# Performance work log

Hardware: AMD Instinct MI355X
Metric: run time of the kernel (lower is better)

## Reference

```python
import jax, jax.numpy as jnp
import numpy as np

H = 1024
NH = 16
HD = H // NH  # 64


def setup_inputs() -> dict:
    key = jax.random.key(0)
    ks = jax.random.split(key, 7)
    s = 1.0 / np.sqrt(H)
    return {
        "hidden_states": jax.random.normal(ks[0], (4, 2048, H), dtype=jnp.float32),
        "Wq": jax.random.normal(ks[1], (H, H), dtype=jnp.float32) * s,
        "bq": jnp.zeros((H,), dtype=jnp.float32),
        "Wk": jax.random.normal(ks[2], (H, H), dtype=jnp.float32) * s,
        "bk": jnp.zeros((H,), dtype=jnp.float32),
        "Wv": jax.random.normal(ks[3], (H, H), dtype=jnp.float32) * s,
        "bv": jnp.zeros((H,), dtype=jnp.float32),
    }


def _split_heads(x):
    # [B,S,H] -> [B,NH,S,HD]
    b, s, _ = x.shape
    return x.reshape(b, s, NH, HD).transpose(0, 2, 1, 3)


def reference(hidden_states, Wq, bq, Wk, bk, Wv, bv):
    q = _split_heads(hidden_states @ Wq + bq)
    k = _split_heads(hidden_states @ Wk + bk)
    v = _split_heads(hidden_states @ Wv + bv)
    scores = jnp.einsum("bhqd,bhkd->bhqk", q, k) / jnp.sqrt(jnp.float32(HD))
    probs = jax.nn.softmax(scores, axis=-1)  # dropout p=0 (eval) -> identity
    ctx = jnp.einsum("bhqk,bhkd->bhqd", probs, v)
    b, _, s, _ = ctx.shape
    return ctx.transpose(0, 2, 1, 3).reshape(b, s, H)
```

## Files before the change

### kernel.cpp

```cpp
#include <hip/hip_runtime.h>
#include <hip/hip_bf16.h>

#define BB  4
#define SS  2048
#define HH  1024
#define NHH 16
#define HDD 64

typedef unsigned short u16;
typedef unsigned int   u32;
using bf16x8 = __attribute__((ext_vector_type(8))) short;
using f32x4  = __attribute__((ext_vector_type(4))) float;
using f32x16 = __attribute__((ext_vector_type(16))) float;
using u32x4  = __attribute__((ext_vector_type(4))) u32;

#define SBAR()   asm volatile("s_barrier" ::: "memory")
#define WAITV0() asm volatile("s_waitcnt vmcnt(0)" ::: "memory")
#define WAITV4() asm volatile("s_waitcnt vmcnt(4)" ::: "memory")
#define WAITV8() asm volatile("s_waitcnt vmcnt(8)" ::: "memory")
#define SCHEDB() __builtin_amdgcn_sched_barrier(0)

__device__ __forceinline__ u16 f2b(float f) {
    union { float f; u32 u; } x; x.f = f;
    return (u16)((x.u + 0x7fffu + ((x.u >> 16) & 1u)) >> 16);
}

__device__ __forceinline__ void gload16(const u16* g, u16* l) {
    __builtin_amdgcn_global_load_lds(
        (const __attribute__((address_space(1))) void*)g,
        (__attribute__((address_space(3))) void*)l, 16, 0, 0);
}

__global__ __launch_bounds__(256) void conv(
    const float* __restrict__ X,
    const float* __restrict__ Wq, const float* __restrict__ Wk,
    const float* __restrict__ Wv,
    u16* __restrict__ Xb, u16* __restrict__ Wt)
{
    const int bid = blockIdx.x;
    const int t = threadIdx.x;
    if (bid < 4096) {
        const int i = bid * 256 + t;
        float4 a = ((const float4*)X)[i * 2];
        float4 b = ((const float4*)X)[i * 2 + 1];
        ushort4 s0, s1;
        s0.x = f2b(a.x); s0.y = f2b(a.y); s0.z = f2b(a.z); s0.w = f2b(a.w);
        s1.x = f2b(b.x); s1.y = f2b(b.y); s1.z = f2b(b.z); s1.w = f2b(b.w);
        ((ushort4*)Xb)[i * 2] = s0;
        ((ushort4*)Xb)[i * 2 + 1] = s1;
        return;
    }
    const int idx = bid - 4096;
    const int z = idx >> 10, rem = idx & 1023;
    const int k0 = (rem >> 5) * 32, n0 = (rem & 31) * 32;
    const float* W = (z == 0) ? Wq : (z == 1) ? Wk : Wv;
    u16* out = Wt + (size_t)z * HH * HH;
    __shared__ float T[32][33];
    {
        const int kl = t >> 3, n4 = (t & 7) * 4;
        float4 v = *(const float4*)&W[(size_t)(k0 + kl) * HH + n0 + n4];
        T[n4 + 0][kl] = v.x; T[n4 + 1][kl] = v.y;
        T[n4 + 2][kl] = v.z; T[n4 + 3][kl] = v.w;
    }
    __syncthreads();
    {
        const int nl = t >> 3, k4 = (t & 7) * 4;
        ushort4 s;
        s.x = f2b(T[nl][k4 + 0]); s.y = f2b(T[nl][k4 + 1]);
        s.z = f2b(T[nl][k4 + 2]); s.w = f2b(T[nl][k4 + 3]);
        *(ushort4*)&out[(size_t)(n0 + nl) * HH + k0 + k4] = s;
    }
}

__global__ __launch_bounds__(256, 2) void qkv_gemm(
    const u16* __restrict__ Xb, const u16* __restrict__ Wtb,
    const float* __restrict__ bq, const float* __restrict__ bk,
    const float* __restrict__ bv,
    u16* __restrict__ Qw, u16* __restrict__ Kw, u16* __restrict__ Vw)
{
    const int z  = blockIdx.z;
    const float* bias = (z == 0) ? bq : (z == 1) ? bk : bv;
    const int m0 = blockIdx.x * 128, n0 = blockIdx.y * 128;

    __shared__ __align__(16) u16 Xs[2][128 * 64];
    __shared__ __align__(16) u16 Ws[2][128 * 64];

    const int t = threadIdx.x;
    const int w = t >> 6, lane = t & 63, lr = lane & 15, quad = lane >> 4;
    const int l3 = lane >> 3, c7 = lane & 7;
    const int cl = (c7 ^ l3) * 8;
    const int wm = w >> 1, wn = w & 1;

    const u16* Wtz = Wtb + (size_t)z * HH * HH;

    f32x4 acc[4][4];
    #pragma unroll
    for (int i = 0; i < 4; i++)
        #pragma unroll
        for (int j = 0; j < 4; j++) acc[i][j] = f32x4{0.f, 0.f, 0.f, 0.f};

    #pragma unroll
    for (int e = 0; e < 4; e++) {
        const int r = w * 32 + e * 8 + l3;
        gload16(&Xb [(size_t)(m0 + r) * HH + cl], &Xs[0][(w * 32 + e * 8) * 64]);
        gload16(&Wtz[(size_t)(n0 + r) * HH + cl], &Ws[0][(w * 32 + e * 8) * 64]);
    }

    for (int kt = 0; kt < 16; kt++) {
        const int cur = kt & 1;
        if (kt < 15) {
            const int k0 = (kt + 1) * 64;
            #pragma unroll
            for (int e = 0; e < 4; e++) {
                const int r = w * 32 + e * 8 + l3;
                gload16(&Xb [(size_t)(m0 + r) * HH + k0 + cl],
                        &Xs[cur ^ 1][(w * 32 + e * 8) * 64]);
                gload16(&Wtz[(size_t)(n0 + r) * HH + k0 + cl],
                        &Ws[cur ^ 1][(w * 32 + e * 8) * 64]);
            }
            WAITV8();
        } else {
            WAITV0();
        }
        SBAR();
        SCHEDB();

        #pragma unroll
        for (int kc = 0; kc < 2; kc++) {
            bf16x8 af[4], bfr[4];
            const int ph = ((kc * 4 + quad) ^ c7) * 8;
            #pragma unroll
            for (int mi = 0; mi < 4; mi++)
                af[mi] = *(const bf16x8*)&Xs[cur][(wm * 64 + mi * 16 + lr) * 64 + ph];
            #pragma unroll
            for (int ni = 0; ni < 4; ni++)
                bfr[ni] = *(const bf16x8*)&Ws[cur][(wn * 64 + ni * 16 + lr) * 64 + ph];
            if (z != 2) {
                #pragma unroll
                for (int mi = 0; mi < 4; mi++)
                    #pragma unroll
                    for (int ni = 0; ni < 4; ni++)
                        acc[mi][ni] = __builtin_amdgcn_mfma_f32_16x16x32_bf16(
                            bfr[ni], af[mi], acc[mi][ni], 0, 0, 0);
            } else {
                #pragma unroll
                for (int mi = 0; mi < 4; mi++)
                    #pragma unroll
                    for (int ni = 0; ni < 4; ni++)
                        acc[mi][ni] = __builtin_amdgcn_mfma_f32_16x16x32_bf16(
                            af[mi], bfr[ni], acc[mi][ni], 0, 0, 0);
            }
        }
        SCHEDB();
        SBAR();
    }

    if (z != 2) {
        u16* dst = (z == 0) ? Qw : Kw;
        const float cs = (z == 0) ? 0.18033688011112042f : 1.0f;
        #pragma unroll
        for (int mi = 0; mi < 4; mi++) {
            const int sg = m0 + wm * 64 + mi * 16 + lr;
            const int b = sg >> 11, s = sg & 2047;
            #pragma unroll
            for (int ni = 0; ni < 4; ni++) {
                const int nb = n0 + wn * 64 + ni * 16 + quad * 4;
                const int h = nb >> 6, d0 = nb & 63;
                float4 bb4 = *(const float4*)&bias[nb];
                ushort4 vs;
                vs.x = f2b((acc[mi][ni][0] + bb4.x) * cs);
                vs.y = f2b((acc[mi][ni][1] + bb4.y) * cs);
                vs.z = f2b((acc[mi][ni][2] + bb4.z) * cs);
                vs.w = f2b((acc[mi][ni][3] + bb4.w) * cs);
                *(ushort4*)&dst[((size_t)(b * NHH + h) * SS + s) * HDD + d0] = vs;
            }
        }
    } else {
        #pragma unroll
        for (int mi = 0; mi < 4; mi++)
            #pragma unroll
            for (int ni = 0; ni < 4; ni++) {
                const int mb = m0 + wm * 64 + mi * 16 + quad * 4;
                const int b = mb >> 11, s0 = mb & 2047;
                const int n = n0 + wn * 64 + ni * 16 + lr;
                const int h = n >> 6, d = n & 63;
                const float bv4 = bias[n];
                ushort4 vs;
                vs.x = f2b(acc[mi][ni][0] + bv4);
                vs.y = f2b(acc[mi][ni][1] + bv4);
                vs.z = f2b(acc[mi][ni][2] + bv4);
                vs.w = f2b(acc[mi][ni][3] + bv4);
                *(ushort4*)&Vw[((size_t)(b * NHH + h) * HDD + d) * SS + s0] = vs;
            }
    }
}

struct PU { union { u32x4 u; bf16x8 v; }; };

__device__ __forceinline__ void packHalf(const f32x16& s, PU* pa, float& lsum) {
    float p[16];
    #pragma unroll
    for (int r = 0; r < 16; r++) p[r] = __builtin_amdgcn_exp2f(s[r]);
    lsum += ((((p[0] + p[1]) + (p[2] + p[3]))
            + ((p[4] + p[5]) + (p[6] + p[7])))
           + (((p[8] + p[9]) + (p[10] + p[11]))
            + ((p[12] + p[13]) + (p[14] + p[15]))));
    u32 x0, x1, x2, x3, y0, y1, y2, y3;
    asm("v_cvt_pk_bf16_f32 %0, %1, %2" : "=v"(x0) : "v"(p[0]),  "v"(p[1]));
    asm("v_cvt_pk_bf16_f32 %0, %1, %2" : "=v"(x1) : "v"(p[2]),  "v"(p[3]));
    asm("v_cvt_pk_bf16_f32 %0, %1, %2" : "=v"(y0) : "v"(p[4]),  "v"(p[5]));
    asm("v_cvt_pk_bf16_f32 %0, %1, %2" : "=v"(y1) : "v"(p[6]),  "v"(p[7]));
    asm("v_cvt_pk_bf16_f32 %0, %1, %2" : "=v"(x2) : "v"(p[8]),  "v"(p[9]));
    asm("v_cvt_pk_bf16_f32 %0, %1, %2" : "=v"(x3) : "v"(p[10]), "v"(p[11]));
    asm("v_cvt_pk_bf16_f32 %0, %1, %2" : "=v"(y2) : "v"(p[12]), "v"(p[13]));
    asm("v_cvt_pk_bf16_f32 %0, %1, %2" : "=v"(y3) : "v"(p[14]), "v"(p[15]));
    asm("v_permlane32_swap_b32 %0, %1" : "+v"(x0), "+v"(y0));
    asm("v_permlane32_swap_b32 %0, %1" : "+v"(x1), "+v"(y1));
    asm("v_permlane32_swap_b32 %0, %1" : "+v"(x2), "+v"(y2));
    asm("v_permlane32_swap_b32 %0, %1" : "+v"(x3), "+v"(y3));
    pa[0].u = u32x4{x0, x1, y0, y1};
    pa[1].u = u32x4{x2, x3, y2, y3};
}

__global__ __launch_bounds__(256, 2) void attn(
    const u16* __restrict__ Qb, const u16* __restrict__ Kb,
    const u16* __restrict__ Vtb, float* __restrict__ Out)
{
    const int bid = blockIdx.x;
    const int hh = bid & 63, qt = bid >> 6;
    const int b = hh >> 4, h = hh & 15;
    const size_t hb = (size_t)hh * SS * HDD;

    __shared__ __align__(16) u16 Ks[2][64 * 64];
    __shared__ __align__(16) u16 Vs[2][64 * 64];

    const int t = threadIdx.x;
    const int w = t >> 6, lane = t & 63;
    const int q32 = lane & 31, hi = lane >> 5;
    const int l3 = lane >> 3, c7 = lane & 7;
    const int cl = (c7 ^ l3) * 8;

    bf16x8 qfA[4], qfB[4];
    {
        const size_t qrA = (size_t)(qt * 256 + w * 64 + q32);
        #pragma unroll
        for (int ds = 0; ds < 4; ds++) {
            qfA[ds] = *(const bf16x8*)&Qb[hb + qrA * HDD + ds * 16 + hi * 8];
            qfB[ds] = *(const bf16x8*)&Qb[hb + (qrA + 32) * HDD + ds * 16 + hi * 8];
        }
    }
    asm volatile("" :: "v"(qfA[0]), "v"(qfA[1]), "v"(qfA[2]), "v"(qfA[3]),
                       "v"(qfB[0]), "v"(qfB[1]), "v"(qfB[2]), "v"(qfB[3]));

    {
        const int r0 = w * 16 + l3, r1 = r0 + 8;
        gload16(&Kb [hb + (size_t)r0 * HDD + cl], &Ks[0][(w * 16) * 64]);
        gload16(&Kb [hb + (size_t)r1 * HDD + cl], &Ks[0][(w * 16 + 8) * 64]);
        gload16(&Vtb[hb + (size_t)r0 * SS + cl],  &Vs[0][(w * 16) * 64]);
        gload16(&Vtb[hb + (size_t)r1 * SS + cl],  &Vs[0][(w * 16 + 8) * 64]);
    }

    float lsA = 0.f, lsB = 0.f;
    f32x16 oA0 = {}, oA1 = {}, oB0 = {}, oB1 = {};

    for (int kt = 0; kt < SS / 64; kt++) {
        const int bb = kt & 1;
        if (kt + 1 < SS / 64) {
            const int r0 = w * 16 + l3, r1 = r0 + 8;
            gload16(&Kb [hb + (size_t)((kt + 1) * 64 + r0) * HDD + cl],
                    &Ks[bb ^ 1][(w * 16) * 64]);
            gload16(&Kb [hb + (size_t)((kt + 1) * 64 + r1) * HDD + cl],
                    &Ks[bb ^ 1][(w * 16 + 8) * 64]);
            gload16(&Vtb[hb + (size_t)r0 * SS + (kt + 1) * 64 + cl],
                    &Vs[bb ^ 1][(w * 16) * 64]);
            gload16(&Vtb[hb + (size_t)r1 * SS + (kt + 1) * 64 + cl],
                    &Vs[bb ^ 1][(w * 16 + 8) * 64]);
            WAITV4();
        } else {
            WAITV0();
        }
        SBAR();
        SCHEDB();

        f32x16 sA0 = {}, sB0 = {};
        __builtin_amdgcn_s_setprio(1);
        #pragma unroll
        for (int ds = 0; ds < 4; ds++) {
            const int ph = ((ds * 2 + hi) ^ c7) * 8;
            bf16x8 kf = *(const bf16x8*)&Ks[bb][q32 * 64 + ph];
            sA0 = __builtin_amdgcn_mfma_f32_32x32x16_bf16(kf, qfA[ds], sA0, 0, 0, 0);
            sB0 = __builtin_amdgcn_mfma_f32_32x32x16_bf16(kf, qfB[ds], sB0, 0, 0, 0);
        }
        f32x16 sA1 = {}, sB1 = {};
        #pragma unroll
        for (int ds = 0; ds < 4; ds++) {
            const int ph = ((ds * 2 + hi) ^ c7) * 8;
            bf16x8 kf = *(const bf16x8*)&Ks[bb][(32 + q32) * 64 + ph];
            sA1 = __builtin_amdgcn_mfma_f32_32x32x16_bf16(kf, qfA[ds], sA1, 0, 0, 0);
            sB1 = __builtin_amdgcn_mfma_f32_32x32x16_bf16(kf, qfB[ds], sB1, 0, 0, 0);
        }
        __builtin_amdgcn_s_setprio(0);

        PU paA[4], paB[4];
        packHalf(sA0, &paA[0], lsA);
        packHalf(sB0, &paB[0], lsB);

        __builtin_amdgcn_s_setprio(1);
        #pragma unroll
        for (int ks = 0; ks < 2; ks++) {
            const int ph = ((ks * 2 + hi) ^ c7) * 8;
            bf16x8 vf0 = *(const bf16x8*)&Vs[bb][q32 * 64 + ph];
            bf16x8 vf1 = *(const bf16x8*)&Vs[bb][(32 + q32) * 64 + ph];
            oA0 = __builtin_amdgcn_mfma_f32_32x32x16_bf16(paA[ks].v, vf0, oA0, 0, 0, 0);
            oA1 = __builtin_amdgcn_mfma_f32_32x32x16_bf16(paA[ks].v, vf1, oA1, 0, 0, 0);
            oB0 = __builtin_amdgcn_mfma_f32_32x32x16_bf16(paB[ks].v, vf0, oB0, 0, 0, 0);
            oB1 = __builtin_amdgcn_mfma_f32_32x32x16_bf16(paB[ks].v, vf1, oB1, 0, 0, 0);
        }
        __builtin_amdgcn_s_setprio(0);

        packHalf(sA1, &paA[2], lsA);
        packHalf(sB1, &paB[2], lsB);

        __builtin_amdgcn_s_setprio(1);
        #pragma unroll
        for (int ks = 2; ks < 4; ks++) {
            const int ph = ((ks * 2 + hi) ^ c7) * 8;
            bf16x8 vf0 = *(const bf16x8*)&Vs[bb][q32 * 64 + ph];
            bf16x8 vf1 = *(const bf16x8*)&Vs[bb][(32 + q32) * 64 + ph];
            oA0 = __builtin_amdgcn_mfma_f32_32x32x16_bf16(paA[ks].v, vf0, oA0, 0, 0, 0);
            oA1 = __builtin_amdgcn_mfma_f32_32x32x16_bf16(paA[ks].v, vf1, oA1, 0, 0, 0);
            oB0 = __builtin_amdgcn_mfma_f32_32x32x16_bf16(paB[ks].v, vf0, oB0, 0, 0, 0);
            oB1 = __builtin_amdgcn_mfma_f32_32x32x16_bf16(paB[ks].v, vf1, oB1, 0, 0, 0);
        }
        __builtin_amdgcn_s_setprio(0);

        SCHEDB();
        SBAR();
    }

    lsA += __shfl_xor(lsA, 32);
    lsB += __shfl_xor(lsB, 32);
    const float invA = 1.0f / lsA, invB = 1.0f / lsB;

    #pragma unroll
    for (int r = 0; r < 16; r++) {
        const int cr = (r & 3) + 8 * (r >> 2) + 4 * hi;
        const float iA = __shfl(invA, cr);
        const float iB = __shfl(invB, cr);
        const int rqA = qt * 256 + w * 64 + cr;
        float* oA = &Out[((size_t)(b * SS + rqA)) * HH + h * HDD + q32];
        oA[0]  = oA0[r] * iA;
        oA[32] = oA1[r] * iA;
        float* oB = &Out[((size_t)(b * SS + rqA + 32)) * HH + h * HDD + q32];
        oB[0]  = oB0[r] * iB;
        oB[32] = oB1[r] * iB;
    }
}

extern "C" void kernel_launch(void* const* d_in, const int* in_sizes, int n_in,
                              void* d_out, int out_size, void* d_ws, size_t ws_size,
                              hipStream_t stream) {
    const float* X  = (const float*)d_in[0];
    const float* Wq = (const float*)d_in[1];
    const float* bq = (const float*)d_in[2];
    const float* Wk = (const float*)d_in[3];
    const float* bk = (const float*)d_in[4];
    const float* Wv = (const float*)d_in[5];
    const float* bv = (const float*)d_in[6];
    float* Out = (float*)d_out;

    const size_t elems = (size_t)BB * SS * HH;
    u16* Qw = (u16*)d_ws;
    u16* Kw = Qw + elems;
    u16* Vw = Kw + elems;
    u16* Xb = (u16*)d_out;
    u16* Wt = Xb + elems;

    conv<<<dim3(4096 + 3072), 256, 0, stream>>>(X, Wq, Wk, Wv, Xb, Wt);
    qkv_gemm<<<dim3(64, 8, 3), 256, 0, stream>>>(Xb, Wt, bq, bk, bv, Qw, Kw, Vw);
    attn<<<dim3(512), 256, 0, stream>>>(Qw, Kw, Vw, Out);
}
```

Baseline: 245.2 us.

## Enlarge QKV GEMM tiles to 256x256 with 8 waves and interleaved staged prefetch

New measurement: 505.0 us. 2.06x slower.

```diff
diff --git a/kernel.cpp b/kernel.cpp
--- a/kernel.cpp
+++ b/kernel.cpp
@@ -16,8 +16,9 @@
 
 #define SBAR()   asm volatile("s_barrier" ::: "memory")
 #define WAITV0() asm volatile("s_waitcnt vmcnt(0)" ::: "memory")
+#define WAITV2() asm volatile("s_waitcnt vmcnt(2)" ::: "memory")
 #define WAITV4() asm volatile("s_waitcnt vmcnt(4)" ::: "memory")
-#define WAITV8() asm volatile("s_waitcnt vmcnt(8)" ::: "memory")
+#define LGKM0()  asm volatile("s_waitcnt lgkmcnt(0)" ::: "memory")
 #define SCHEDB() __builtin_amdgcn_sched_barrier(0)
 
 __device__ __forceinline__ u16 f2b(float f) {
@@ -72,7 +73,7 @@
     }
 }
 
-__global__ __launch_bounds__(256, 2) void qkv_gemm(
+__global__ __launch_bounds__(512, 2) void qkv_gemm(
     const u16* __restrict__ Xb, const u16* __restrict__ Wtb,
     const float* __restrict__ bq, const float* __restrict__ bk,
     const float* __restrict__ bv,
@@ -80,78 +81,159 @@
 {
     const int z  = blockIdx.z;
     const float* bias = (z == 0) ? bq : (z == 1) ? bk : bv;
-    const int m0 = blockIdx.x * 128, n0 = blockIdx.y * 128;
-
-    __shared__ __align__(16) u16 Xs[2][128 * 64];
-    __shared__ __align__(16) u16 Ws[2][128 * 64];
+    const int m0 = blockIdx.x * 256, n0 = blockIdx.y * 256;
+
+    __shared__ __align__(16) u16 As[2][256 * 64];
+    __shared__ __align__(16) u16 Bs[2][256 * 64];
 
     const int t = threadIdx.x;
     const int w = t >> 6, lane = t & 63, lr = lane & 15, quad = lane >> 4;
     const int l3 = lane >> 3, c7 = lane & 7;
     const int cl = (c7 ^ l3) * 8;
-    const int wm = w >> 1, wn = w & 1;
+    const int wm = w >> 2, wn = w & 3;
 
     const u16* Wtz = Wtb + (size_t)z * HH * HH;
 
-    f32x4 acc[4][4];
+    auto stage = [&](int h, int kt, int nb) {
+        const int rbase = (h & 1) * 128 + w * 16;
+        const int k0 = kt * 64;
+        if (h < 2) {
+            gload16(&Xb[(size_t)(m0 + rbase + l3) * HH + k0 + cl],
+                    &As[nb][rbase * 64]);
+            gload16(&Xb[(size_t)(m0 + rbase + 8 + l3) * HH + k0 + cl],
+                    &As[nb][(rbase + 8) * 64]);
+        } else {
+            gload16(&Wtz[(size_t)(n0 + rbase + l3) * HH + k0 + cl],
+                    &Bs[nb][rbase * 64]);
+            gload16(&Wtz[(size_t)(n0 + rbase + 8 + l3) * HH + k0 + cl],
+                    &Bs[nb][(rbase + 8) * 64]);
+        }
+    };
+
+    f32x4 acc[8][4];
     #pragma unroll
-    for (int i = 0; i < 4; i++)
+    for (int i = 0; i < 8; i++)
         #pragma unroll
         for (int j = 0; j < 4; j++) acc[i][j] = f32x4{0.f, 0.f, 0.f, 0.f};
 
-    #pragma unroll
-    for (int e = 0; e < 4; e++) {
-        const int r = w * 32 + e * 8 + l3;
-        gload16(&Xb [(size_t)(m0 + r) * HH + cl], &Xs[0][(w * 32 + e * 8) * 64]);
-        gload16(&Wtz[(size_t)(n0 + r) * HH + cl], &Ws[0][(w * 32 + e * 8) * 64]);
-    }
+    stage(0, 0, 0); stage(1, 0, 0); stage(2, 0, 0); stage(3, 0, 0);
+
+    bf16x8 af[8], bf[2];
 
     for (int kt = 0; kt < 16; kt++) {
-        const int cur = kt & 1;
-        if (kt < 15) {
-            const int k0 = (kt + 1) * 64;
-            #pragma unroll
-            for (int e = 0; e < 4; e++) {
-                const int r = w * 32 + e * 8 + l3;
-                gload16(&Xb [(size_t)(m0 + r) * HH + k0 + cl],
-                        &Xs[cur ^ 1][(w * 32 + e * 8) * 64]);
-                gload16(&Wtz[(size_t)(n0 + r) * HH + k0 + cl],
-                        &Ws[cur ^ 1][(w * 32 + e * 8) * 64]);
-            }
-            WAITV8();
-        } else {
-            WAITV0();
-        }
-        SBAR();
-        SCHEDB();
-
-        #pragma unroll
-        for (int kc = 0; kc < 2; kc++) {
-            bf16x8 af[4], bfr[4];
-            const int ph = ((kc * 4 + quad) ^ c7) * 8;
-            #pragma unroll
-            for (int mi = 0; mi < 4; mi++)
-                af[mi] = *(const bf16x8*)&Xs[cur][(wm * 64 + mi * 16 + lr) * 64 + ph];
-            #pragma unroll
-            for (int ni = 0; ni < 4; ni++)
-                bfr[ni] = *(const bf16x8*)&Ws[cur][(wn * 64 + ni * 16 + lr) * 64 + ph];
-            if (z != 2) {
-                #pragma unroll
-                for (int mi = 0; mi < 4; mi++)
-                    #pragma unroll
-                    for (int ni = 0; ni < 4; ni++)
-                        acc[mi][ni] = __builtin_amdgcn_mfma_f32_16x16x32_bf16(
-                            bfr[ni], af[mi], acc[mi][ni], 0, 0, 0);
-            } else {
-                #pragma unroll
-                for (int mi = 0; mi < 4; mi++)
-                    #pragma unroll
-                    for (int ni = 0; ni < 4; ni++)
-                        acc[mi][ni] = __builtin_amdgcn_mfma_f32_16x16x32_bf16(
-                            af[mi], bfr[ni], acc[mi][ni], 0, 0, 0);
-            }
-        }
-        SCHEDB();
+        const int c = kt & 1, nb = c ^ 1;
+        const bool pf = (kt < 15);
+
+        if (pf) { stage(0, kt + 1, nb); WAITV2(); } else { WAITV0(); }
+        SBAR();
+        #pragma unroll
+        for (int mi = 0; mi < 8; mi++)
+            af[mi] = *(const bf16x8*)&As[c][(wm * 128 + mi * 16 + lr) * 64
+                                            + (quad ^ c7) * 8];
+        #pragma unroll
+        for (int j = 0; j < 2; j++)
+            bf[j] = *(const bf16x8*)&Bs[c][(wn * 64 + j * 16 + lr) * 64
+                                           + (quad ^ c7) * 8];
+        LGKM0(); SCHEDB();
+        __builtin_amdgcn_s_setprio(1);
+        if (z != 2) {
+            #pragma unroll
+            for (int mi = 0; mi < 8; mi++)
+                #pragma unroll
+                for (int j = 0; j < 2; j++)
+                    acc[mi][j] = __builtin_amdgcn_mfma_f32_16x16x32_bf16(
+                        bf[j], af[mi], acc[mi][j], 0, 0, 0);
+        } else {
+            #pragma unroll
+            for (int mi = 0; mi < 8; mi++)
+                #pragma unroll
+                for (int j = 0; j < 2; j++)
+                    acc[mi][j] = __builtin_amdgcn_mfma_f32_16x16x32_bf16(
+                        af[mi], bf[j], acc[mi][j], 0, 0, 0);
+        }
+        __builtin_amdgcn_s_setprio(0);
+        SBAR();
+
+        if (pf) stage(1, kt + 1, nb);
+        #pragma unroll
+        for (int j = 0; j < 2; j++)
+            bf[j] = *(const bf16x8*)&Bs[c][(wn * 64 + (2 + j) * 16 + lr) * 64
+                                           + (quad ^ c7) * 8];
+        SBAR();
+        LGKM0(); SCHEDB();
+        __builtin_amdgcn_s_setprio(1);
+        if (z != 2) {
+            #pragma unroll
+            for (int mi = 0; mi < 8; mi++)
+                #pragma unroll
+                for (int j = 0; j < 2; j++)
+                    acc[mi][2 + j] = __builtin_amdgcn_mfma_f32_16x16x32_bf16(
+                        bf[j], af[mi], acc[mi][2 + j], 0, 0, 0);
+        } else {
+            #pragma unroll
+            for (int mi = 0; mi < 8; mi++)
+                #pragma unroll
+                for (int j = 0; j < 2; j++)
+                    acc[mi][2 + j] = __builtin_amdgcn_mfma_f32_16x16x32_bf16(
+                        af[mi], bf[j], acc[mi][2 + j], 0, 0, 0);
+        }
+        __builtin_amdgcn_s_setprio(0);
+        SBAR();
+
+        if (pf) stage(2, kt + 1, nb);
+        #pragma unroll
+        for (int mi = 0; mi < 8; mi++)
+            af[mi] = *(const bf16x8*)&As[c][(wm * 128 + mi * 16 + lr) * 64
+                                            + ((4 + quad) ^ c7) * 8];
+        #pragma unroll
+        for (int j = 0; j < 2; j++)
+            bf[j] = *(const bf16x8*)&Bs[c][(wn * 64 + j * 16 + lr) * 64
+                                           + ((4 + quad) ^ c7) * 8];
+        SBAR();
+        LGKM0(); SCHEDB();
+        __builtin_amdgcn_s_setprio(1);
+        if (z != 2) {
+            #pragma unroll
+            for (int mi = 0; mi < 8; mi++)
+                #pragma unroll
+                for (int j = 0; j < 2; j++)
+                    acc[mi][j] = __builtin_amdgcn_mfma_f32_16x16x32_bf16(
+                        bf[j], af[mi], acc[mi][j], 0, 0, 0);
+        } else {
+            #pragma unroll
+            for (int mi = 0; mi < 8; mi++)
+                #pragma unroll
+                for (int j = 0; j < 2; j++)
+                    acc[mi][j] = __builtin_amdgcn_mfma_f32_16x16x32_bf16(
+                        af[mi], bf[j], acc[mi][j], 0, 0, 0);
+        }
+        __builtin_amdgcn_s_setprio(0);
+        SBAR();
+
+        if (pf) stage(3, kt + 1, nb);
+        #pragma unroll
+        for (int j = 0; j < 2; j++)
+            bf[j] = *(const bf16x8*)&Bs[c][(wn * 64 + (2 + j) * 16 + lr) * 64
+                                           + ((4 + quad) ^ c7) * 8];
+        SBAR();
+        LGKM0(); SCHEDB();
+        __builtin_amdgcn_s_setprio(1);
+        if (z != 2) {
+            #pragma unroll
+            for (int mi = 0; mi < 8; mi++)
+                #pragma unroll
+                for (int j = 0; j < 2; j++)
+                    acc[mi][2 + j] = __builtin_amdgcn_mfma_f32_16x16x32_bf16(
+                        bf[j], af[mi], acc[mi][2 + j], 0, 0, 0);
+        } else {
+            #pragma unroll
+            for (int mi = 0; mi < 8; mi++)
+                #pragma unroll
+                for (int j = 0; j < 2; j++)
+                    acc[mi][2 + j] = __builtin_amdgcn_mfma_f32_16x16x32_bf16(
+                        af[mi], bf[j], acc[mi][2 + j], 0, 0, 0);
+        }
+        __builtin_amdgcn_s_setprio(0);
         SBAR();
     }
 
@@ -159,37 +241,37 @@
         u16* dst = (z == 0) ? Qw : Kw;
         const float cs = (z == 0) ? 0.18033688011112042f : 1.0f;
         #pragma unroll
-        for (int mi = 0; mi < 4; mi++) {
-            const int sg = m0 + wm * 64 + mi * 16 + lr;
+        for (int mi = 0; mi < 8; mi++) {
+            const int sg = m0 + wm * 128 + mi * 16 + lr;
             const int b = sg >> 11, s = sg & 2047;
             #pragma unroll
-            for (int ni = 0; ni < 4; ni++) {
-                const int nb = n0 + wn * 64 + ni * 16 + quad * 4;
-                const int h = nb >> 6, d0 = nb & 63;
-                float4 bb4 = *(const float4*)&bias[nb];
+            for (int nf = 0; nf < 4; nf++) {
+                const int nb2 = n0 + wn * 64 + nf * 16 + quad * 4;
+                const int h = nb2 >> 6, d0 = nb2 & 63;
+                float4 bb4 = *(const float4*)&bias[nb2];
                 ushort4 vs;
-                vs.x = f2b((acc[mi][ni][0] + bb4.x) * cs);
-                vs.y = f2b((acc[mi][ni][1] + bb4.y) * cs);
-                vs.z = f2b((acc[mi][ni][2] + bb4.z) * cs);
-                vs.w = f2b((acc[mi][ni][3] + bb4.w) * cs);
+                vs.x = f2b((acc[mi][nf][0] + bb4.x) * cs);
+                vs.y = f2b((acc[mi][nf][1] + bb4.y) * cs);
+                vs.z = f2b((acc[mi][nf][2] + bb4.z) * cs);
+                vs.w = f2b((acc[mi][nf][3] + bb4.w) * cs);
                 *(ushort4*)&dst[((size_t)(b * NHH + h) * SS + s) * HDD + d0] = vs;
             }
         }
     } else {
         #pragma unroll
-        for (int mi = 0; mi < 4; mi++)
-            #pragma unroll
-            for (int ni = 0; ni < 4; ni++) {
-                const int mb = m0 + wm * 64 + mi * 16 + quad * 4;
+        for (int mi = 0; mi < 8; mi++)
+            #pragma unroll
+            for (int nf = 0; nf < 4; nf++) {
+                const int mb = m0 + wm * 128 + mi * 16 + quad * 4;
                 const int b = mb >> 11, s0 = mb & 2047;
-                const int n = n0 + wn * 64 + ni * 16 + lr;
+                const int n = n0 + wn * 64 + nf * 16 + lr;
                 const int h = n >> 6, d = n & 63;
                 const float bv4 = bias[n];
                 ushort4 vs;
-                vs.x = f2b(acc[mi][ni][0] + bv4);
-                vs.y = f2b(acc[mi][ni][1] + bv4);
-                vs.z = f2b(acc[mi][ni][2] + bv4);
-                vs.w = f2b(acc[mi][ni][3] + bv4);
+                vs.x = f2b(acc[mi][nf][0] + bv4);
+                vs.y = f2b(acc[mi][nf][1] + bv4);
+                vs.z = f2b(acc[mi][nf][2] + bv4);
+                vs.w = f2b(acc[mi][nf][3] + bv4);
                 *(ushort4*)&Vw[((size_t)(b * NHH + h) * HDD + d) * SS + s0] = vs;
             }
     }
@@ -377,6 +459,6 @@
     u16* Wt = Xb + elems;
 
     conv<<<dim3(4096 + 3072), 256, 0, stream>>>(X, Wq, Wk, Wv, Xb, Wt);
-    qkv_gemm<<<dim3(64, 8, 3), 256, 0, stream>>>(Xb, Wt, bq, bk, bv, Qw, Kw, Vw);
+    qkv_gemm<<<dim3(32, 4, 3), 512, 0, stream>>>(Xb, Wt, bq, bk, bv, Qw, Kw, Vw);
     attn<<<dim3(512), 256, 0, stream>>>(Qw, Kw, Vw, Out);
 }
```
